# Kernel optimization log

Hardware: AMD Instinct MI355X
Metric: run time of the kernel (lower is better)

The kernel has to match this reference:

```python
import jax, jax.numpy as jnp
import numpy as np

L, DIN, D, NL = 16384, 256, 768, 8
EPS = 1e-5


def _ln(x, g, b):
    mu = jnp.mean(x, axis=-1, keepdims=True)
    var = jnp.mean(jnp.square(x - mu), axis=-1, keepdims=True)
    return (x - mu) * jax.lax.rsqrt(var + EPS) * g + b


def setup_inputs() -> dict:
    key = jax.random.key(0)
    ks = iter(jax.random.split(key, 24))
    nrm = lambda shape, s=0.02: jax.random.normal(next(ks), shape, jnp.float32) * s
    return {
        "node_features": jax.random.normal(next(ks), (L, DIN), jnp.float32),
        "W_proj": nrm((DIN, D)), "b_proj": jnp.zeros((D,), jnp.float32),
        "ln_s_g": jnp.ones((NL, D), jnp.float32), "ln_s_b": jnp.zeros((NL, D), jnp.float32),
        "W_in": nrm((NL, D, D)), "b_in": jnp.zeros((NL, D), jnp.float32),
        "W_gate": nrm((NL, D, D)), "b_gate": jnp.zeros((NL, D), jnp.float32),
        "W_out": nrm((NL, D, D)), "b_out": jnp.zeros((NL, D), jnp.float32),
        "decay_logit": nrm((NL, D), 0.5),
        "ln_f_g": jnp.ones((NL, D), jnp.float32), "ln_f_b": jnp.zeros((NL, D), jnp.float32),
        "W_ff1": nrm((NL, D, 2 * D)), "b_ff1": jnp.zeros((NL, 2 * D), jnp.float32),
        "W_ff2": nrm((NL, 2 * D, D)), "b_ff2": jnp.zeros((NL, D), jnp.float32),
        "ln_o_g": jnp.ones((D,), jnp.float32), "ln_o_b": jnp.zeros((D,), jnp.float32),
    }


def reference(node_features, W_proj, b_proj, ln_s_g, ln_s_b, W_in, b_in,
              W_gate, b_gate, W_out, b_out, decay_logit, ln_f_g, ln_f_b,
              W_ff1, b_ff1, W_ff2, b_ff2, ln_o_g, ln_o_b):
    x = node_features @ W_proj + b_proj  # [L, D]
    for l in range(NL):
        h = _ln(x, ln_s_g[l], ln_s_b[l])
        u = h @ W_in[l] + b_in[l]                      # [L, D]
        gate = jax.nn.sigmoid(h @ W_gate[l] + b_gate[l])
        decay = jax.nn.sigmoid(decay_logit[l])         # [D]

        def step(state, u_t):
            state = decay * state + u_t
            return state, state

        _, states = jax.lax.scan(step, jnp.zeros((D,), x.dtype), u)  # [L, D]
        x = x + (states * gate) @ W_out[l] + b_out[l]
        hf = _ln(x, ln_f_g[l], ln_f_b[l])
        x = x + jax.nn.silu(hf @ W_ff1[l] + b_ff1[l]) @ W_ff2[l] + b_ff2[l]
    return _ln(x, ln_o_g, ln_o_b)
```

## Files before the change

### kernel.cpp

```cpp
#include <hip/hip_runtime.h>
#include <hip/hip_bf16.h>
#include <math.h>
#include <string.h>

#define L_TOK 16384
#define D_INP 256
#define D_MOD 768
#define D_FF  1536
#define N_LAYER 8
#define S_T 16
#define S_G 1024
#define S_SB 32
#define EPSV 1e-5f

typedef short bf16x8 __attribute__((ext_vector_type(8)));
typedef float f32x4 __attribute__((ext_vector_type(4)));
typedef __hip_bfloat16 bf16;
typedef unsigned int u32;
typedef unsigned short u16;

__device__ __forceinline__ float fsigmoid(float z) { return 1.0f / (1.0f + __expf(-z)); }

__device__ __forceinline__ u16 f2bf(float f) {
  __hip_bfloat16 h = __float2bfloat16(f);
  u16 r; memcpy(&r, &h, 2); return r;
}
__device__ __forceinline__ float bf2f(u16 v) {
  u32 x = ((u32)v) << 16; float f; memcpy(&f, &x, 4); return f;
}

__device__ __forceinline__ void glds16(const short* g, short* l) {
  __builtin_amdgcn_global_load_lds(
      (const __attribute__((address_space(1))) unsigned int*)(g),
      (__attribute__((address_space(3))) unsigned int*)(l), 16, 0, 0);
}

__device__ __forceinline__ bf16x8 dsr128(const char* base, int imm) {
  bf16x8 r;
  const __attribute__((address_space(3))) char* p =
      (const __attribute__((address_space(3))) char*)base;
  asm volatile("ds_read_b128 %0, %1 offset:%c2" : "=v"(r) : "v"(p), "i"(imm));
  return r;
}

__global__ void k_f32_to_bf16v(const float4* __restrict__ src, ushort4* __restrict__ dst, int n4) {
  int i = blockIdx.x * blockDim.x + threadIdx.x;
  if (i < n4) {
    float4 v = src[i];
    ushort4 o; o.x = f2bf(v.x); o.y = f2bf(v.y); o.z = f2bf(v.z); o.w = f2bf(v.w);
    dst[i] = o;
  }
}

template<bool FOLD>
__global__ void k_transpose_fold(const float* __restrict__ src, bf16* __restrict__ dst,
                                 int R, int C, size_t sstride, size_t dstride,
                                 const float* __restrict__ gv, const float* __restrict__ bv,
                                 float* __restrict__ wacc, float* __restrict__ bacc,
                                 int vstride) {
  __shared__ float tile[32][33];
  int z = blockIdx.z;
  const float* s = src + (size_t)z * sstride;
  bf16* d = dst + (size_t)z * dstride;
  int r0 = blockIdx.y * 32, c0 = blockIdx.x * 32;
  int tx = threadIdx.x, ty = threadIdx.y;
#pragma unroll
  for (int i = ty; i < 32; i += 8)
    tile[i][tx] = s[(size_t)(r0 + i) * C + (c0 + tx)];
  __syncthreads();
  float gk = 1.0f;
  if (FOLD) gk = gv[(size_t)z * R + r0 + tx];
#pragma unroll
  for (int i = ty; i < 32; i += 8) {
    float val = tile[tx][i];
    if (FOLD) val *= gk;
    d[(size_t)(c0 + i) * R + (r0 + tx)] = __float2bfloat16(val);
  }
  if (FOLD && ty == 0) {
    const float* gz = gv + (size_t)z * R + r0;
    const float* bz = bv + (size_t)z * R + r0;
    float s1 = 0.f, s2 = 0.f;
#pragma unroll 8
    for (int j = 0; j < 32; j++) {
      float wv = tile[j][tx];
      s1 += gz[j] * wv;
      s2 += bz[j] * wv;
    }
    atomicAdd(&wacc[(size_t)z * vstride + c0 + tx], s1);
    atomicAdd(&bacc[(size_t)z * vstride + c0 + tx], s2);
  }
}

template<int MODE, bool LNFOLD, bool STATS>
__global__ __launch_bounds__(256, 4) void k_gemm128(
    const short* __restrict__ A, const short* __restrict__ Bt,
    const float* __restrict__ bias, const float* __restrict__ bias2,
    const float* __restrict__ wvec, const float* __restrict__ bvec,
    const float* __restrict__ stats_in, float* __restrict__ stats_out,
    u16* __restrict__ res, u16* __restrict__ outp, u16* __restrict__ outp2,
    int N, int K, int ncol)
{
  __shared__ short As[2][128 * 32];
  __shared__ short Bs[2][128 * 32];
  __shared__ float s_mu[128], s_rv[128];
  const int tid = threadIdx.x;
  const int lane = tid & 63, w = tid >> 6;
  const int wr = w >> 1, wc = w & 1;
  const int l16 = lane & 15, qd = lane >> 4;

  const int b = blockIdx.x;
  const int xcd = b & 7, t = b >> 3;
  const int m0 = (xcd * 16 + t / ncol) * 128;
  const int n0 = (t % ncol) * 128;

  const int sr = lane >> 2, sc = lane & 3;
  const int ar = w * 32 + sr;
  const int acx = sc ^ ((ar >> 1) & 3);
  const short* ag0 = A  + (size_t)(m0 + ar) * K + acx * 8;
  const short* ag1 = ag0 + (size_t)16 * K;
  const short* bg0 = Bt + (size_t)(n0 + ar) * K + acx * 8;
  const short* bg1 = bg0 + (size_t)16 * K;

  auto stg = [&](int bi, int k0) {
    short* a0 = &As[bi][w * 1024];
    glds16(ag0 + k0, a0); glds16(ag1 + k0, a0 + 512);
    short* b0 = &Bs[bi][w * 1024];
    glds16(bg0 + k0, b0); glds16(bg1 + k0, b0 + 512);
  };

  const int fo = (qd ^ ((l16 >> 1) & 3)) * 8 + l16 * 32;

  float sv = 0.f, sq = 0.f;
  if (LNFOLD && tid < 128) {
    sv = stats_in[2 * (m0 + tid)];
    sq = stats_in[2 * (m0 + tid) + 1];
  }

  const int NT = K >> 5;
  stg(0, 0);

  if (LNFOLD && tid < 128) {
    float mu  = sv * (1.0f / (float)D_MOD);
    float var = sq * (1.0f / (float)D_MOD) - mu * mu;
    s_mu[tid] = mu;
    s_rv[tid] = 1.0f / sqrtf(var + EPSV);
  }

  f32x4 acc[4][4];
#pragma unroll
  for (int i = 0; i < 4; i++)
#pragma unroll
    for (int j = 0; j < 4; j++) acc[i][j] = (f32x4){0.f, 0.f, 0.f, 0.f};

  asm volatile("s_waitcnt vmcnt(0)" ::: "memory");
  __builtin_amdgcn_s_barrier();

  for (int t2 = 0; t2 < NT; ++t2) {
    const int rd = t2 & 1;
    if (t2 + 1 < NT) stg(rd ^ 1, (t2 + 1) * 32);
    const char* ab = (const char*)&As[rd][wr * 2048 + fo];
    const char* bb2 = (const char*)&Bs[rd][wc * 2048 + fo];
    bf16x8 af0 = dsr128(ab, 0),    af1 = dsr128(ab, 1024);
    bf16x8 af2 = dsr128(ab, 2048), af3 = dsr128(ab, 3072);
    bf16x8 bf0 = dsr128(bb2, 0),    bf1 = dsr128(bb2, 1024);
    bf16x8 bf2 = dsr128(bb2, 2048), bf3 = dsr128(bb2, 3072);
    asm volatile("s_waitcnt lgkmcnt(0)" ::: "memory");
    __builtin_amdgcn_sched_barrier(0);
    bf16x8 af[4] = {af0, af1, af2, af3};
    bf16x8 bfr[4] = {bf0, bf1, bf2, bf3};
#pragma unroll
    for (int rt = 0; rt < 4; rt++)
#pragma unroll
      for (int ct = 0; ct < 4; ct++)
        acc[rt][ct] = __builtin_amdgcn_mfma_f32_16x16x32_bf16(af[rt], bfr[ct], acc[rt][ct], 0, 0, 0);
    asm volatile("s_waitcnt vmcnt(0)" ::: "memory");
    __builtin_amdgcn_s_barrier();
  }

  const float* bb = bias;
  u16* op = outp;
  int nofs = 0, Nout = N;
  bool sig = false;
  if (MODE == 4) {
    Nout = N >> 1;
    if (n0 >= Nout) { bb = bias2; op = outp2; nofs = Nout; sig = true; }
  }
  const int gmb = m0 + wr * 64 + qd * 4;
  const int gnb = n0 + wc * 64 + l16;
  float bc[4], wv4[4], bv4[4];
#pragma unroll
  for (int ct = 0; ct < 4; ct++) {
    int gn = gnb + ct * 16;
    bc[ct] = bb[gn - nofs];
    if (LNFOLD) { wv4[ct] = wvec[gn]; bv4[ct] = bvec[gn]; }
  }
#pragma unroll
  for (int rt = 0; rt < 4; rt++) {
#pragma unroll
    for (int r = 0; r < 4; r++) {
      const int gm = gmb + rt * 16 + r;
      float mu = 0.f, rv = 0.f;
      if (LNFOLD) { mu = s_mu[gm - m0]; rv = s_rv[gm - m0]; }
      float ps = 0.f, ps2 = 0.f;
#pragma unroll
      for (int ct = 0; ct < 4; ct++) {
        int gn = gnb + ct * 16;
        float vv = acc[rt][ct][r];
        if (LNFOLD) vv = rv * vv - rv * mu * wv4[ct] + bv4[ct] + bc[ct];
        else        vv += bc[ct];
        if (MODE == 2) vv = vv * fsigmoid(vv);
        if (MODE == 4 && sig) vv = fsigmoid(vv);
        size_t oidx = (size_t)gm * Nout + (gn - nofs);
        if (MODE == 3) vv += bf2f(res[oidx]);
        u16 rb = f2bf(vv);
        op[oidx] = rb;
        if (STATS) { float fv = bf2f(rb); ps += fv; ps2 += fv * fv; }
      }
      if (STATS) {
#pragma unroll
        for (int o = 1; o < 16; o <<= 1) {
          ps  += __shfl_xor(ps, o, 64);
          ps2 += __shfl_xor(ps2, o, 64);
        }
        if (l16 == 0) {
          atomicAdd(&stats_out[2 * gm], ps);
          atomicAdd(&stats_out[2 * gm + 1], ps2);
        }
      }
    }
  }
}

__global__ void k_scan_a(const bf16* __restrict__ u, const float* __restrict__ dl,
                         float* __restrict__ clast) {
  int t = threadIdx.x;
  int g = blockIdx.x;
  int d0 = t * 4;
  float dec[4], s[4] = {0.f, 0.f, 0.f, 0.f};
#pragma unroll
  for (int c = 0; c < 4; c++) dec[c] = fsigmoid(dl[d0 + c]);
  const ushort4* up = (const ushort4*)(u + (size_t)g * S_T * D_MOD) + t;
  ushort4 nxt = up[0];
#pragma unroll 4
  for (int tt = 0; tt < S_T; tt++) {
    ushort4 uv = nxt;
    if (tt + 1 < S_T) nxt = up[(size_t)(tt + 1) * 192];
    s[0] = fmaf(dec[0], s[0], bf2f(uv.x));
    s[1] = fmaf(dec[1], s[1], bf2f(uv.y));
    s[2] = fmaf(dec[2], s[2], bf2f(uv.z));
    s[3] = fmaf(dec[3], s[3], bf2f(uv.w));
  }
#pragma unroll
  for (int c = 0; c < 4; c++) clast[(size_t)g * D_MOD + d0 + c] = s[c];
}

__global__ void k_scan_b1(const float* __restrict__ clast, const float* __restrict__ dl,
                          float* __restrict__ inner, float* __restrict__ sbsum) {
  int d = threadIdx.x;
  int sb = blockIdx.x;
  float dec = fsigmoid(dl[d]);
  float aT = dec;
#pragma unroll
  for (int i = 0; i < 4; i++) aT *= aT;
  const float* cp = clast + (size_t)sb * 32 * D_MOD + d;
  float* ip = inner + (size_t)sb * 32 * D_MOD + d;
  float c = 0.f;
#pragma unroll
  for (int j = 0; j < 32; j++) {
    ip[(size_t)j * D_MOD] = c;
    c = fmaf(aT, c, cp[(size_t)j * D_MOD]);
  }
  sbsum[(size_t)sb * D_MOD + d] = c;
}

__global__ void k_scan_b2(const float* __restrict__ sbsum, const float* __restrict__ dl,
                          float* __restrict__ sbcarry) {
  int d = threadIdx.x;
  float dec = fsigmoid(dl[d]);
  float A = dec;
#pragma unroll
  for (int i = 0; i < 9; i++) A *= A;
  float c = 0.f;
#pragma unroll
  for (int sb = 0; sb < 32; sb++) {
    sbcarry[(size_t)sb * D_MOD + d] = c;
    c = fmaf(A, c, sbsum[(size_t)sb * D_MOD + d]);
  }
}

__global__ void k_scan_c(const bf16* __restrict__ u, const float* __restrict__ dl,
                         const float* __restrict__ inner, const float* __restrict__ sbcarry,
                         bf16* __restrict__ gate_s) {
  int t = threadIdx.x;
  int g = blockIdx.x;
  int d0 = t * 4;
  float dec[4], s[4];
#pragma unroll
  for (int c = 0; c < 4; c++) dec[c] = fsigmoid(dl[d0 + c]);
  {
    float4 iv = *(const float4*)(inner + (size_t)g * D_MOD + d0);
    float4 sv = *(const float4*)(sbcarry + (size_t)(g >> 5) * D_MOD + d0);
    int e = g & 31;
    float pw[4], bs[4];
#pragma unroll
    for (int c = 0; c < 4; c++) {
      float aT = dec[c];
#pragma unroll
      for (int i = 0; i < 4; i++) aT *= aT;
      pw[c] = 1.f; bs[c] = aT;
    }
#pragma unroll
    for (int bit = 0; bit < 5; bit++) {
      if ((e >> bit) & 1) {
#pragma unroll
        for (int c = 0; c < 4; c++) pw[c] *= bs[c];
      }
#pragma unroll
      for (int c = 0; c < 4; c++) bs[c] *= bs[c];
    }
    s[0] = fmaf(pw[0], sv.x, iv.x);
    s[1] = fmaf(pw[1], sv.y, iv.y);
    s[2] = fmaf(pw[2], sv.z, iv.z);
    s[3] = fmaf(pw[3], sv.w, iv.w);
  }
  const ushort4* up = (const ushort4*)(u + (size_t)g * S_T * D_MOD) + t;
  ushort4* gp = (ushort4*)(gate_s + (size_t)g * S_T * D_MOD) + t;
  ushort4 nu = up[0], ng = gp[0];
#pragma unroll 4
  for (int tt = 0; tt < S_T; tt++) {
    ushort4 uv = nu, gv = ng;
    if (tt + 1 < S_T) {
      nu = up[(size_t)(tt + 1) * 192];
      ng = gp[(size_t)(tt + 1) * 192];
    }
    s[0] = fmaf(dec[0], s[0], bf2f(uv.x));
    s[1] = fmaf(dec[1], s[1], bf2f(uv.y));
    s[2] = fmaf(dec[2], s[2], bf2f(uv.z));
    s[3] = fmaf(dec[3], s[3], bf2f(uv.w));
    ushort4 ov;
    ov.x = f2bf(s[0] * bf2f(gv.x));
    ov.y = f2bf(s[1] * bf2f(gv.y));
    ov.z = f2bf(s[2] * bf2f(gv.z));
    ov.w = f2bf(s[3] * bf2f(gv.w));
    gp[(size_t)tt * 192] = ov;
  }
}

__global__ __launch_bounds__(256) void k_ln_final(const u16* __restrict__ x,
    const float* __restrict__ stats, const float* __restrict__ g,
    const float* __restrict__ b, float* __restrict__ outp) {
  int wv = threadIdx.x >> 6, lane = threadIdx.x & 63;
  int row = blockIdx.x * 4 + wv;
  float sv = stats[2 * row], sq = stats[2 * row + 1];
  float mu = sv * (1.0f / (float)D_MOD);
  float var = sq * (1.0f / (float)D_MOD) - mu * mu;
  float rv = 1.0f / sqrtf(var + EPSV);
  const ushort4* xr = (const ushort4*)(x + (size_t)row * D_MOD);
  const float4* g4 = (const float4*)g;
  const float4* b4 = (const float4*)b;
  float4* o4 = (float4*)(outp + (size_t)row * D_MOD);
#pragma unroll
  for (int j = 0; j < 3; j++) {
    int f = j * 64 + lane;
    ushort4 xv = xr[f];
    float4 gg = g4[f], bb = b4[f], ov;
    ov.x = (bf2f(xv.x) - mu) * rv * gg.x + bb.x;
    ov.y = (bf2f(xv.y) - mu) * rv * gg.y + bb.y;
    ov.z = (bf2f(xv.z) - mu) * rv * gg.z + bb.z;
    ov.w = (bf2f(xv.w) - mu) * rv * gg.w + bb.w;
    o4[f] = ov;
  }
}

extern "C" void kernel_launch(void* const* d_in, const int* in_sizes, int n_in,
                              void* d_out, int out_size, void* d_ws, size_t ws_size,
                              hipStream_t stream) {
  const float* nf     = (const float*)d_in[0];
  const float* W_proj = (const float*)d_in[1];
  const float* b_proj = (const float*)d_in[2];
  const float* ln_s_g = (const float*)d_in[3];
  const float* ln_s_b = (const float*)d_in[4];
  const float* W_in   = (const float*)d_in[5];
  const float* b_in   = (const float*)d_in[6];
  const float* W_gate = (const float*)d_in[7];
  const float* b_gate = (const float*)d_in[8];
  const float* W_out  = (const float*)d_in[9];
  const float* b_out  = (const float*)d_in[10];
  const float* dlogit = (const float*)d_in[11];
  const float* ln_f_g = (const float*)d_in[12];
  const float* ln_f_b = (const float*)d_in[13];
  const float* W_ff1  = (const float*)d_in[14];
  const float* b_ff1  = (const float*)d_in[15];
  const float* W_ff2  = (const float*)d_in[16];
  const float* b_ff2  = (const float*)d_in[17];
  const float* ln_o_g = (const float*)d_in[18];
  const float* ln_o_b = (const float*)d_in[19];
  (void)in_sizes; (void)n_in;

  char* ws = (char*)d_ws;
  size_t off = 0;
  auto alloc = [&](size_t bytes) -> char* {
    char* p = ws + off;
    off = (off + bytes + 255) & ~(size_t)255;
    return p;
  };
  const bool big = ws_size >= (160ull << 20);
  const size_t wmul = big ? N_LAYER : 1;

  u16*   x     = (u16*)alloc(2ull * L_TOK * D_MOD);
  char*  ug    = alloc(2ull * L_TOK * D_FF);
  u16*   u     = (u16*)ug;
  u16*   gate  = (u16*)(ug + 2ull * L_TOK * D_MOD);
  u16*   tb    = (u16*)ug;
  u16*   nfb   = (u16*)ug;
  bf16*  WprojT= (bf16*)alloc(2ull * D_INP * D_MOD);
  bf16*  WigT  = (bf16*)alloc(2ull * wmul * (2 * D_MOD) * D_MOD);
  bf16*  WoT   = (bf16*)alloc(2ull * wmul * D_MOD * D_MOD);
  bf16*  Wff1T = (bf16*)alloc(2ull * wmul * D_MOD * D_FF);
  bf16*  Wff2T = (bf16*)alloc(2ull * wmul * D_FF * D_MOD);
  float* clast = (float*)alloc(sizeof(float) * (size_t)S_G * D_MOD);
  float* carry = (float*)alloc(sizeof(float) * (size_t)S_G * D_MOD);
  float* sbsum = (float*)alloc(sizeof(float) * (size_t)S_SB * D_MOD);
  float* sbcar = (float*)alloc(sizeof(float) * (size_t)S_SB * D_MOD);
  char*  zbase = alloc(0);
  float* stats = (float*)alloc(sizeof(float) * 17ull * L_TOK * 2);
  float* wvig  = (float*)alloc(sizeof(float) * N_LAYER * 2 * D_MOD);
  float* bvig  = (float*)alloc(sizeof(float) * N_LAYER * 2 * D_MOD);
  float* wvf1  = (float*)alloc(sizeof(float) * N_LAYER * D_FF);
  float* bvf1  = (float*)alloc(sizeof(float) * N_LAYER * D_FF);
  size_t zbytes = (size_t)((char*)ws + off - zbase);
  hipMemsetAsync(zbase, 0, zbytes, stream);

  const size_t DD = (size_t)D_MOD * D_MOD, DF = (size_t)D_MOD * D_FF;
  auto statslot = [&](int s) { return stats + (size_t)s * L_TOK * 2; };
  dim3 tb32(32, 8);
  k_f32_to_bf16v<<<(L_TOK * D_INP / 4 + 255) / 256, 256, 0, stream>>>(
      (const float4*)nf, (ushort4*)nfb, L_TOK * D_INP / 4);
  k_transpose_fold<false><<<dim3(D_MOD / 32, D_INP / 32, 1), tb32, 0, stream>>>(
      W_proj, WprojT, D_INP, D_MOD, 0, 0, nullptr, nullptr, nullptr, nullptr, 0);
  if (big) {
    k_transpose_fold<true><<<dim3(D_MOD / 32, D_MOD / 32, N_LAYER), tb32, 0, stream>>>(
        W_in,   WigT,      D_MOD, D_MOD, DD, 2 * DD, ln_s_g, ln_s_b, wvig,       bvig,       2 * D_MOD);
    k_transpose_fold<true><<<dim3(D_MOD / 32, D_MOD / 32, N_LAYER), tb32, 0, stream>>>(
        W_gate, WigT + DD, D_MOD, D_MOD, DD, 2 * DD, ln_s_g, ln_s_b, wvig + D_MOD, bvig + D_MOD, 2 * D_MOD);
    k_transpose_fold<false><<<dim3(D_MOD / 32, D_MOD / 32, N_LAYER), tb32, 0, stream>>>(
        W_out,  WoT,       D_MOD, D_MOD, DD, DD, nullptr, nullptr, nullptr, nullptr, 0);
    k_transpose_fold<true><<<dim3(D_FF / 32,  D_MOD / 32, N_LAYER), tb32, 0, stream>>>(
        W_ff1,  Wff1T,     D_MOD, D_FF,  DF, DF, ln_f_g, ln_f_b, wvf1, bvf1, D_FF);
    k_transpose_fold<false><<<dim3(D_MOD / 32, D_FF / 32,  N_LAYER), tb32, 0, stream>>>(
        W_ff2,  Wff2T,     D_FF,  D_MOD, DF, DF, nullptr, nullptr, nullptr, nullptr, 0);
  }

  k_gemm128<0, false, true><<<128 * 6, 256, 0, stream>>>(
      (const short*)nfb, (const short*)WprojT, b_proj, nullptr, nullptr, nullptr,
      nullptr, statslot(0), nullptr, x, nullptr, D_MOD, D_INP, 6);

  for (int l = 0; l < N_LAYER; l++) {
    const bf16 *wigT, *woT, *wf1T, *wf2T;
    if (big) {
      wigT = WigT  + (size_t)l * 2 * DD;
      woT  = WoT   + (size_t)l * DD;
      wf1T = Wff1T + (size_t)l * DF;
      wf2T = Wff2T + (size_t)l * DF;
    } else {
      k_transpose_fold<true><<<dim3(D_MOD / 32, D_MOD / 32, 1), tb32, 0, stream>>>(
          W_in + (size_t)l * DD, WigT, D_MOD, D_MOD, 0, 0,
          ln_s_g + l * D_MOD, ln_s_b + l * D_MOD, wvig + (size_t)l * 2 * D_MOD, bvig + (size_t)l * 2 * D_MOD, 0);
      k_transpose_fold<true><<<dim3(D_MOD / 32, D_MOD / 32, 1), tb32, 0, stream>>>(
          W_gate + (size_t)l * DD, WigT + DD, D_MOD, D_MOD, 0, 0,
          ln_s_g + l * D_MOD, ln_s_b + l * D_MOD, wvig + (size_t)l * 2 * D_MOD + D_MOD, bvig + (size_t)l * 2 * D_MOD + D_MOD, 0);
      k_transpose_fold<false><<<dim3(D_MOD / 32, D_MOD / 32, 1), tb32, 0, stream>>>(
          W_out + (size_t)l * DD, WoT, D_MOD, D_MOD, 0, 0, nullptr, nullptr, nullptr, nullptr, 0);
      k_transpose_fold<true><<<dim3(D_FF / 32, D_MOD / 32, 1), tb32, 0, stream>>>(
          W_ff1 + (size_t)l * DF, Wff1T, D_MOD, D_FF, 0, 0,
          ln_f_g + l * D_MOD, ln_f_b + l * D_MOD, wvf1 + (size_t)l * D_FF, bvf1 + (size_t)l * D_FF, 0);
      k_transpose_fold<false><<<dim3(D_MOD / 32, D_FF / 32, 1), tb32, 0, stream>>>(
          W_ff2 + (size_t)l * DF, Wff2T, D_FF, D_MOD, 0, 0, nullptr, nullptr, nullptr, nullptr, 0);
      wigT = WigT; woT = WoT; wf1T = Wff1T; wf2T = Wff2T;
    }

    k_gemm128<4, true, false><<<128 * 12, 256, 0, stream>>>(
        (const short*)x, (const short*)wigT, b_in + l * D_MOD, b_gate + l * D_MOD,
        wvig + (size_t)l * 2 * D_MOD, bvig + (size_t)l * 2 * D_MOD,
        statslot(2 * l), nullptr, nullptr, u, gate, 2 * D_MOD, D_MOD, 12);
    k_scan_a<<<S_G, 192, 0, stream>>>((const bf16*)u, dlogit + l * D_MOD, clast);
    k_scan_b1<<<S_G / 32, D_MOD, 0, stream>>>(clast, dlogit + l * D_MOD, carry, sbsum);
    k_scan_b2<<<1, D_MOD, 0, stream>>>(sbsum, dlogit + l * D_MOD, sbcar);
    k_scan_c<<<S_G, 192, 0, stream>>>((const bf16*)u, dlogit + l * D_MOD, carry, sbcar, (bf16*)gate);
    k_gemm128<3, false, true><<<128 * 6, 256, 0, stream>>>(
        (const short*)gate, (const short*)woT, b_out + l * D_MOD, nullptr, nullptr, nullptr,
        nullptr, statslot(2 * l + 1), x, x, nullptr, D_MOD, D_MOD, 6);
    k_gemm128<2, true, false><<<128 * 12, 256, 0, stream>>>(
        (const short*)x, (const short*)wf1T, b_ff1 + l * D_FF, nullptr,
        wvf1 + (size_t)l * D_FF, bvf1 + (size_t)l * D_FF,
        statslot(2 * l + 1), nullptr, nullptr, tb, nullptr, D_FF, D_MOD, 12);
    k_gemm128<3, false, true><<<128 * 6, 256, 0, stream>>>(
        (const short*)tb, (const short*)wf2T, b_ff2 + l * D_MOD, nullptr, nullptr, nullptr,
        nullptr, statslot(2 * l + 2), x, x, nullptr, D_MOD, D_FF, 6);
  }

  k_ln_final<<<L_TOK / 4, 256, 0, stream>>>(x, statslot(2 * N_LAYER), ln_o_g, ln_o_b, (float*)d_out);
}
```

Measured before the change: 2.142 ms.

## Fuse scan chunk-local reduction into the in/gate GEMM epilogue

The first phase of the chunked linear scan (per-16-token chunk end states) is now computed inside the in/gate GEMM epilogue. Each lane weights its accumulator values by powers of the decay and reduces across the quad lanes with shuffles, then writes clast directly. This removes the separate k_scan_a kernel and its re-read of u from global memory each layer. In exchange the GEMM epilogue gains extra registers and arithmetic, and the sums now use different decay-power weighting and ordering.

```diff
diff --git a/kernel.cpp b/kernel.cpp
--- a/kernel.cpp
+++ b/kernel.cpp
@@ -91,13 +91,14 @@
   }
 }
 
-template<int MODE, bool LNFOLD, bool STATS>
+template<int MODE, bool LNFOLD, bool STATS, bool FSCAN>
 __global__ __launch_bounds__(256, 4) void k_gemm128(
     const short* __restrict__ A, const short* __restrict__ Bt,
     const float* __restrict__ bias, const float* __restrict__ bias2,
     const float* __restrict__ wvec, const float* __restrict__ bvec,
     const float* __restrict__ stats_in, float* __restrict__ stats_out,
     u16* __restrict__ res, u16* __restrict__ outp, u16* __restrict__ outp2,
+    const float* __restrict__ dlog, float* __restrict__ clast_out,
     int N, int K, int ncol)
 {
   __shared__ short As[2][128 * 32];
@@ -194,8 +195,23 @@
     bc[ct] = bb[gn - nofs];
     if (LNFOLD) { wv4[ct] = wvec[gn]; bv4[ct] = bvec[gn]; }
   }
+  float dec1[4], dec2[4], dec3[4], qdb[4];
+  if (FSCAN && !sig) {
+#pragma unroll
+    for (int ct = 0; ct < 4; ct++) {
+      int gn = gnb + ct * 16;
+      float dv = fsigmoid(dlog[gn]);
+      dec1[ct] = dv;
+      dec2[ct] = dv * dv;
+      dec3[ct] = dec2[ct] * dv;
+      float d4 = dec2[ct] * dec2[ct];
+      float d8 = d4 * d4, d12 = d8 * d4;
+      qdb[ct] = (qd == 0) ? d12 : (qd == 1) ? d8 : (qd == 2) ? d4 : 1.0f;
+    }
+  }
 #pragma unroll
   for (int rt = 0; rt < 4; rt++) {
+    float cs[4] = {0.f, 0.f, 0.f, 0.f};
 #pragma unroll
     for (int r = 0; r < 4; r++) {
       const int gm = gmb + rt * 16 + r;
@@ -215,6 +231,11 @@
         u16 rb = f2bf(vv);
         op[oidx] = rb;
         if (STATS) { float fv = bf2f(rb); ps += fv; ps2 += fv * fv; }
+        if (FSCAN && !sig) {
+          float fv = bf2f(rb);
+          float wp = (r == 0) ? dec3[ct] : (r == 1) ? dec2[ct] : (r == 2) ? dec1[ct] : 1.0f;
+          cs[ct] = fmaf(fv, wp, cs[ct]);
+        }
       }
       if (STATS) {
 #pragma unroll
@@ -228,30 +249,18 @@
         }
       }
     }
-  }
-}
-
-__global__ void k_scan_a(const bf16* __restrict__ u, const float* __restrict__ dl,
-                         float* __restrict__ clast) {
-  int t = threadIdx.x;
-  int g = blockIdx.x;
-  int d0 = t * 4;
-  float dec[4], s[4] = {0.f, 0.f, 0.f, 0.f};
-#pragma unroll
-  for (int c = 0; c < 4; c++) dec[c] = fsigmoid(dl[d0 + c]);
-  const ushort4* up = (const ushort4*)(u + (size_t)g * S_T * D_MOD) + t;
-  ushort4 nxt = up[0];
-#pragma unroll 4
-  for (int tt = 0; tt < S_T; tt++) {
-    ushort4 uv = nxt;
-    if (tt + 1 < S_T) nxt = up[(size_t)(tt + 1) * 192];
-    s[0] = fmaf(dec[0], s[0], bf2f(uv.x));
-    s[1] = fmaf(dec[1], s[1], bf2f(uv.y));
-    s[2] = fmaf(dec[2], s[2], bf2f(uv.z));
-    s[3] = fmaf(dec[3], s[3], bf2f(uv.w));
-  }
-#pragma unroll
-  for (int c = 0; c < 4; c++) clast[(size_t)g * D_MOD + d0 + c] = s[c];
+    if (FSCAN && !sig) {
+      const int cidx = (m0 + wr * 64 + rt * 16) >> 4;
+#pragma unroll
+      for (int ct = 0; ct < 4; ct++) {
+        float c = cs[ct] * qdb[ct];
+        c += __shfl_xor(c, 16, 64);
+        c += __shfl_xor(c, 32, 64);
+        if (qd == 0)
+          clast_out[(size_t)cidx * D_MOD + gnb + ct * 16] = c;
+      }
+    }
+  }
 }
 
 __global__ void k_scan_b1(const float* __restrict__ clast, const float* __restrict__ dl,
@@ -451,9 +460,9 @@
         W_ff2,  Wff2T,     D_FF,  D_MOD, DF, DF, nullptr, nullptr, nullptr, nullptr, 0);
   }
 
-  k_gemm128<0, false, true><<<128 * 6, 256, 0, stream>>>(
+  k_gemm128<0, false, true, false><<<128 * 6, 256, 0, stream>>>(
       (const short*)nfb, (const short*)WprojT, b_proj, nullptr, nullptr, nullptr,
-      nullptr, statslot(0), nullptr, x, nullptr, D_MOD, D_INP, 6);
+      nullptr, statslot(0), nullptr, x, nullptr, nullptr, nullptr, D_MOD, D_INP, 6);
 
   for (int l = 0; l < N_LAYER; l++) {
     const bf16 *wigT, *woT, *wf1T, *wf2T;
@@ -479,24 +488,24 @@
       wigT = WigT; woT = WoT; wf1T = Wff1T; wf2T = Wff2T;
     }
 
-    k_gemm128<4, true, false><<<128 * 12, 256, 0, stream>>>(
+    k_gemm128<4, true, false, true><<<128 * 12, 256, 0, stream>>>(
         (const short*)x, (const short*)wigT, b_in + l * D_MOD, b_gate + l * D_MOD,
         wvig + (size_t)l * 2 * D_MOD, bvig + (size_t)l * 2 * D_MOD,
-        statslot(2 * l), nullptr, nullptr, u, gate, 2 * D_MOD, D_MOD, 12);
-    k_scan_a<<<S_G, 192, 0, stream>>>((const bf16*)u, dlogit + l * D_MOD, clast);
+        statslot(2 * l), nullptr, nullptr, u, gate,
+        dlogit + l * D_MOD, clast, 2 * D_MOD, D_MOD, 12);
     k_scan_b1<<<S_G / 32, D_MOD, 0, stream>>>(clast, dlogit + l * D_MOD, carry, sbsum);
     k_scan_b2<<<1, D_MOD, 0, stream>>>(sbsum, dlogit + l * D_MOD, sbcar);
     k_scan_c<<<S_G, 192, 0, stream>>>((const bf16*)u, dlogit + l * D_MOD, carry, sbcar, (bf16*)gate);
-    k_gemm128<3, false, true><<<128 * 6, 256, 0, stream>>>(
+    k_gemm128<3, false, true, false><<<128 * 6, 256, 0, stream>>>(
         (const short*)gate, (const short*)woT, b_out + l * D_MOD, nullptr, nullptr, nullptr,
-        nullptr, statslot(2 * l + 1), x, x, nullptr, D_MOD, D_MOD, 6);
-    k_gemm128<2, true, false><<<128 * 12, 256, 0, stream>>>(
+        nullptr, statslot(2 * l + 1), x, x, nullptr, nullptr, nullptr, D_MOD, D_MOD, 6);
+    k_gemm128<2, true, false, false><<<128 * 12, 256, 0, stream>>>(
         (const short*)x, (const short*)wf1T, b_ff1 + l * D_FF, nullptr,
         wvf1 + (size_t)l * D_FF, bvf1 + (size_t)l * D_FF,
-        statslot(2 * l + 1), nullptr, nullptr, tb, nullptr, D_FF, D_MOD, 12);
-    k_gemm128<3, false, true><<<128 * 6, 256, 0, stream>>>(
+        statslot(2 * l + 1), nullptr, nullptr, tb, nullptr, nullptr, nullptr, D_FF, D_MOD, 12);
+    k_gemm128<3, false, true, false><<<128 * 6, 256, 0, stream>>>(
         (const short*)tb, (const short*)wf2T, b_ff2 + l * D_MOD, nullptr, nullptr, nullptr,
-        nullptr, statslot(2 * l + 2), x, x, nullptr, D_MOD, D_FF, 6);
+        nullptr, statslot(2 * l + 2), x, x, nullptr, nullptr, nullptr, D_MOD, D_FF, 6);
   }
 
   k_ln_final<<<L_TOK / 4, 256, 0, stream>>>(x, statslot(2 * N_LAYER), ln_o_g, ln_o_b, (float*)d_out);
```

After: 2.101 ms. About the same (-1.9%).
